# Performance work log

Hardware: AMD Instinct MI355X
Metric: run time of the kernel (lower is better)

The kernel has to match this reference:

```python
import jax, jax.numpy as jnp
import numpy as np
from jax import lax

DN = ('NCHW', 'OIHW', 'NCHW')

def conv(x, w, b, stride, pad):
    y = lax.conv_general_dilated(x, w, (stride, stride), [(pad, pad), (pad, pad)], dimension_numbers=DN)
    return y + b[None, :, None, None]

def setup_inputs() -> dict:
    key = jax.random.key(0)
    ks = jax.random.split(key, 16)
    s = 0.05
    inp = {
        'condition': jax.random.normal(ks[0], (16, 1, 256, 256), jnp.float32),
        'w1': jax.random.normal(ks[1], (64, 1, 4, 4), jnp.float32) * s,
        'b1': jnp.zeros((64,), jnp.float32),
        'w2': jax.random.normal(ks[2], (128, 64, 4, 4), jnp.float32) * s,
        'b2': jnp.zeros((128,), jnp.float32),
        'w3': jax.random.normal(ks[3], (128, 128, 3, 3), jnp.float32) * s,
        'b3': jnp.zeros((128,), jnp.float32),
        'r1w1': jax.random.normal(ks[4], (32, 128, 3, 3), jnp.float32) * s,
        'r1b1': jnp.zeros((32,), jnp.float32),
        'r1w2': jax.random.normal(ks[5], (128, 32, 1, 1), jnp.float32) * s,
        'r1b2': jnp.zeros((128,), jnp.float32),
        'r2w1': jax.random.normal(ks[6], (32, 128, 3, 3), jnp.float32) * s,
        'r2b1': jnp.zeros((32,), jnp.float32),
        'r2w2': jax.random.normal(ks[7], (128, 32, 1, 1), jnp.float32) * s,
        'r2b2': jnp.zeros((128,), jnp.float32),
        'wpre': jax.random.normal(ks[8], (4, 128, 1, 1), jnp.float32) * s,
        'bpre': jnp.zeros((4,), jnp.float32),
        'codebook': jax.random.normal(ks[9], (2048, 4), jnp.float32),
    }
    return inp

def reference(condition, w1, b1, w2, b2, w3, b3, r1w1, r1b1, r1w2, r1b2,
              r2w1, r2b1, r2w2, r2b2, wpre, bpre, codebook):
    # --- conv encoder (VQ-VAE standard) ---
    h = jax.nn.relu(conv(condition, w1, b1, 2, 1))   # [B,64,128,128]
    h = jax.nn.relu(conv(h, w2, b2, 2, 1))           # [B,128,64,64]
    h = conv(h, w3, b3, 1, 1)                        # [B,128,64,64]
    # residual stack: 2 blocks of relu->3x3->relu->1x1, residual add
    for wa, ba, wb, bb in ((r1w1, r1b1, r1w2, r1b2), (r2w1, r2b1, r2w2, r2b2)):
        t = conv(jax.nn.relu(h), wa, ba, 1, 1)
        t = conv(jax.nn.relu(t), wb, bb, 1, 0)
        h = h + t
    h = jax.nn.relu(h)
    z = conv(h, wpre, bpre, 1, 0)                    # [B,4,64,64]
    # --- cosine-distance vector quantization ---
    B, D, H, W = z.shape
    zf = jnp.transpose(z, (0, 2, 3, 1)).reshape(-1, D)          # [BHW, D]
    zn = zf / (jnp.linalg.norm(zf, axis=-1, keepdims=True) + 1e-12)
    en = codebook / (jnp.linalg.norm(codebook, axis=-1, keepdims=True) + 1e-12)
    sim = jnp.einsum('nd,kd->nk', zn, en)                       # cosine similarity
    idx = jnp.argmax(sim, axis=-1)                              # nearest code
    q = codebook[idx].reshape(B, H, W, D)
    c = jnp.transpose(q, (0, 3, 1, 2))                          # [B,4,64,64]
    return c
```

## Files before the change

kernel.cpp:

```cpp
#include <hip/hip_runtime.h>
#include <math.h>


typedef short v8s __attribute__((ext_vector_type(8)));
typedef float v4f __attribute__((ext_vector_type(4)));

#define B_OFF 4194304
#define A_OFF 12582912
#define W2_S 0
#define W3_S 393216
#define WR1_S 835584
#define WR2_S 946176
#define WP1_S 1056768
#define WP2_S 1069056

__device__ inline void limb3(float v, unsigned short& h, unsigned short& m,
                             unsigned short& l) {
    unsigned ub = __float_as_uint(v);
    unsigned hb = ub & 0xffff0000u;
    float r1 = v - __uint_as_float(hb);
    unsigned mb = __float_as_uint(r1) & 0xffff0000u;
    float r2 = r1 - __uint_as_float(mb);
    unsigned lb = __float_as_uint(r2) & 0xffff0000u;
    h = (unsigned short)(hb >> 16);
    m = (unsigned short)(mb >> 16);
    l = (unsigned short)(lb >> 16);
}

struct CfgConv2 {
    static constexpr int NC = 8, NT = 4, OC = 128, ICG = 64, IN_H = 128, IN_W = 128;
    static constexpr bool RELU_IN = false, RELU_OUT = true;
    __device__ static void tap(int c, int t, int& ry, int& rx) {
        int py = (c >> 2) & 1, px = (c >> 1) & 1;
        ry = (t >> 1) - py; rx = (t & 1) - px;
    }
    __device__ static void inaddr(int c, int oy, int r, int X,
                                  int& Yg, int& Xg, int& ic0) {
        int py = (c >> 2) & 1, px = (c >> 1) & 1;
        Yg = 2 * (oy + r - 1) + py; Xg = 2 * X + px; ic0 = (c & 1) * 32;
    }
    __device__ static int widx(int c, int t, int oc, int ic) {
        int py = (c >> 2) & 1, px = (c >> 1) & 1, half = c & 1;
        int dy = 2 * (t >> 1) + (1 - py), dx = 2 * (t & 1) + (1 - px);
        return ((oc * 64 + half * 32 + ic) * 4 + dy) * 4 + dx;
    }
};
struct CfgConv3 {
    static constexpr int NC = 4, NT = 9, OC = 128, ICG = 128, IN_H = 64, IN_W = 64;
    static constexpr bool RELU_IN = false, RELU_OUT = false;
    __device__ static void tap(int c, int t, int& ry, int& rx) {
        ry = t / 3 - 1; rx = t % 3 - 1;
    }
    __device__ static void inaddr(int c, int oy, int r, int X,
                                  int& Yg, int& Xg, int& ic0) {
        Yg = oy + r - 1; Xg = X; ic0 = c * 32;
    }
    __device__ static int widx(int c, int t, int oc, int ic) {
        return ((oc * 128 + c * 32 + ic) * 3 + t / 3) * 3 + t % 3;
    }
};
struct CfgRes {
    static constexpr int NC = 4, NT = 9, OC = 32, ICG = 128, IN_H = 64, IN_W = 64;
    __device__ static int widx(int c, int t, int oc, int ic) {
        return ((oc * 128 + c * 32 + ic) * 3 + t / 3) * 3 + t % 3;
    }
};
struct Cfg1x1 {
    static constexpr int NC = 1, NT = 1, OC = 128;
    __device__ static int widx(int c, int t, int oc, int ic) {
        return oc * 32 + ic;
    }
};

template <typename C>
__device__ inline void repack_one(const float* __restrict__ w,
                                  short* __restrict__ dst, int idx) {
    int s  = idx & 31;
    int oc = (idx >> 5) % C::OC;
    int ct = idx / (32 * C::OC);
    int c = ct / C::NT, t = ct % C::NT;
    float val = w[C::widx(c, t, oc, s)];
    unsigned short h, m, l;
    limb3(val, h, m, l);
    constexpr int NTILE = C::OC / 16;
    int nt = oc >> 4, o = oc & 15, q = s >> 3, j = s & 7;
    int fr = ((q * 16 + o) << 3) + j;
    dst[(((ct * 3 + 0) * NTILE + nt) << 9) + fr] = (short)h;
    dst[(((ct * 3 + 1) * NTILE + nt) << 9) + fr] = (short)m;
    dst[(((ct * 3 + 2) * NTILE + nt) << 9) + fr] = (short)l;
}

__global__ __launch_bounds__(256) void repack_all_k(
    const float* __restrict__ w2, const float* __restrict__ w3,
    const float* __restrict__ r1, const float* __restrict__ r2,
    const float* __restrict__ p1, const float* __restrict__ p2,
    short* __restrict__ base)
{
    int idx = blockIdx.x * 256 + threadIdx.x;
    if (idx < 131072) { repack_one<CfgConv2>(w2, base + W2_S, idx); return; }
    idx -= 131072;
    if (idx < 147456) { repack_one<CfgConv3>(w3, base + W3_S, idx); return; }
    idx -= 147456;
    if (idx < 36864)  { repack_one<CfgRes>(r1, base + WR1_S, idx); return; }
    idx -= 36864;
    if (idx < 36864)  { repack_one<CfgRes>(r2, base + WR2_S, idx); return; }
    idx -= 36864;
    if (idx < 4096)   { repack_one<Cfg1x1>(p1, base + WP1_S, idx); return; }
    idx -= 4096;
    if (idx < 4096)   { repack_one<Cfg1x1>(p2, base + WP2_S, idx); }
}

template <typename C>
__global__ __launch_bounds__(256, 3) void mfma_conv(
    const float* __restrict__ in, const short* __restrict__ repw,
    const float* __restrict__ bias, float* __restrict__ out, int n0)
{
    constexpr int APLANE = 3 * 66 * 32;
    constexpr int NTILE  = C::OC / 16;
    __shared__ __align__(16) short lA[3 * APLANE];

    int tid = threadIdx.x;
    int lane = tid & 63, wv = tid >> 6;
    int n_img = blockIdx.x >> 6, oy = blockIdx.x & 63;

    for (int idx = tid; idx < 3 * 3 * 2 * 16; idx += 256) {
        int plane = idx / 96;
        int rem = idx % 96;
        int rr = rem / 32;
        int hc = (rem / 16) & 1;
        int d = idx & 15;
        ((unsigned*)lA)[plane * 3168 + (rr * 66 + hc * 65) * 16 + d] = 0;
    }

    v4f acc[4][2] = {};
    int nbase = wv * 2;
    int Xq = tid & 15, icp = tid >> 4, quad = lane >> 4;

    float pv[24];
    auto issue_loads = [&](int c) {
#pragma unroll
        for (int it = 0; it < 12; it++) {
            int r = it >> 2, xg = it & 3;
            int X = xg * 16 + Xq;
            int Yg, Xg, ic0;
            C::inaddr(c, oy, r, X, Yg, Xg, ic0);
            float v0 = 0.f, v1 = 0.f;
            if (Yg >= 0 && Yg < C::IN_H) {
                int g = ((n_img * C::ICG + ic0 + 2 * icp) * C::IN_H + Yg) * C::IN_W + Xg;
                v0 = in[g];
                v1 = in[g + C::IN_H * C::IN_W];
            }
            pv[2 * it] = v0; pv[2 * it + 1] = v1;
        }
    };
    auto load_bf = [&](int c, int t, v8s (&dst)[2][3]) {
#pragma unroll
        for (int nt = 0; nt < 2; nt++)
#pragma unroll
            for (int L = 0; L < 3; L++)
                dst[nt][L] = *(const v8s*)(repw +
                    ((((c * C::NT + t) * 3 + L) * NTILE + (nbase + nt)) << 9) +
                    (lane << 3));
    };

    issue_loads(0);

    for (int c = 0; c < C::NC; c++) {
        __syncthreads();
#pragma unroll
        for (int it = 0; it < 12; it++) {
            int r = it >> 2, xg = it & 3;
            int X = xg * 16 + Xq;
            float v0 = pv[2 * it], v1 = pv[2 * it + 1];
            if constexpr (C::RELU_IN) { v0 = fmaxf(v0, 0.f); v1 = fmaxf(v1, 0.f); }
            unsigned short h0, m0, l0, h1, m1, l1;
            limb3(v0, h0, m0, l0);
            limb3(v1, h1, m1, l1);
            int cell = r * 66 + X + 1;
            int f = (cell + (cell >> 2)) & 3;
            int phys = (icp & 3) + 4 * (((icp >> 2) + f) & 3);
            unsigned* pa = (unsigned*)lA + cell * 16 + phys;
            pa[0]        = (unsigned)h0 | ((unsigned)h1 << 16);
            pa[3168]     = (unsigned)m0 | ((unsigned)m1 << 16);
            pa[2 * 3168] = (unsigned)l0 | ((unsigned)l1 << 16);
        }
        __syncthreads();
        if (c + 1 < C::NC) issue_loads(c + 1);

        v8s bf[2][2][3];
        load_bf(c, 0, bf[0]);
#pragma unroll
        for (int t = 0; t < C::NT; t++) {
            constexpr int NTT = C::NT;
            if (t + 1 < NTT) load_bf(c, t + 1, bf[(t + 1) & 1]);
            int ry, rx;
            C::tap(c, t, ry, rx);
#pragma unroll
            for (int mt = 0; mt < 4; mt++) {
                int x = mt * 16 + (lane & 15);
                int cell = (ry + 1) * 66 + (x + rx + 1);
                int f = (cell + (cell >> 2)) & 3;
                int aa = cell * 32 + (((quad + f) & 3) << 3);
                v8s ah = *(const v8s*)&lA[aa];
                v8s am = *(const v8s*)&lA[APLANE + aa];
                v8s al = *(const v8s*)&lA[2 * APLANE + aa];
#pragma unroll
                for (int nt = 0; nt < 2; nt++) {
                    v4f a0 = acc[mt][nt];
                    a0 = __builtin_amdgcn_mfma_f32_16x16x32_bf16(ah, bf[t & 1][nt][0], a0, 0, 0, 0);
                    a0 = __builtin_amdgcn_mfma_f32_16x16x32_bf16(ah, bf[t & 1][nt][1], a0, 0, 0, 0);
                    a0 = __builtin_amdgcn_mfma_f32_16x16x32_bf16(am, bf[t & 1][nt][0], a0, 0, 0, 0);
                    a0 = __builtin_amdgcn_mfma_f32_16x16x32_bf16(am, bf[t & 1][nt][1], a0, 0, 0, 0);
                    a0 = __builtin_amdgcn_mfma_f32_16x16x32_bf16(ah, bf[t & 1][nt][2], a0, 0, 0, 0);
                    a0 = __builtin_amdgcn_mfma_f32_16x16x32_bf16(al, bf[t & 1][nt][0], a0, 0, 0, 0);
                    acc[mt][nt] = a0;
                }
            }
        }
    }
#pragma unroll
    for (int mt = 0; mt < 4; mt++) {
        int x0 = mt * 16 + quad * 4;
#pragma unroll
        for (int nt = 0; nt < 2; nt++) {
            int oc = (nbase + nt) * 16 + (lane & 15);
            float bv = bias[oc];
            float v0 = acc[mt][nt][0] + bv;
            float v1 = acc[mt][nt][1] + bv;
            float v2 = acc[mt][nt][2] + bv;
            float v3 = acc[mt][nt][3] + bv;
            if constexpr (C::RELU_OUT) {
                v0 = fmaxf(v0, 0.f); v1 = fmaxf(v1, 0.f);
                v2 = fmaxf(v2, 0.f); v3 = fmaxf(v3, 0.f);
            }
            float4 o = make_float4(v0, v1, v2, v3);
            *(float4*)&out[(((n0 + n_img) * C::OC + oc) * 64 + oy) * 64 + x0] = o;
        }
    }
}

__global__ __launch_bounds__(256, 4) void mfma_res(
    const float* __restrict__ in, const short* __restrict__ repw,
    const float* __restrict__ b1, const short* __restrict__ repp,
    const float* __restrict__ b2, float* __restrict__ out)
{
    constexpr int APLANE = 3 * 66 * 32;
    __shared__ __align__(16) short lA[3 * APLANE];

    int tid = threadIdx.x;
    int lane = tid & 63, wv = tid >> 6;
    int n_img = blockIdx.x >> 6, oy = blockIdx.x & 63;

    for (int idx = tid; idx < 3 * 3 * 2 * 16; idx += 256) {
        int plane = idx / 96;
        int rem = idx % 96;
        int rr = rem / 32;
        int hc = (rem / 16) & 1;
        int d = idx & 15;
        ((unsigned*)lA)[plane * 3168 + (rr * 66 + hc * 65) * 16 + d] = 0;
    }

    v4f acc[2] = {};
    int Xq = tid & 15, icp = tid >> 4, quad = lane >> 4;

    float pv[24];
    auto issue_loads = [&](int c) {
#pragma unroll
        for (int it = 0; it < 12; it++) {
            int r = it >> 2, xg = it & 3;
            int X = xg * 16 + Xq;
            int Yg = oy + r - 1;
            float v0 = 0.f, v1 = 0.f;
            if (Yg >= 0 && Yg < 64) {
                int g = ((n_img * 128 + c * 32 + 2 * icp) * 64 + Yg) * 64 + X;
                v0 = in[g];
                v1 = in[g + 4096];
            }
            pv[2 * it] = v0; pv[2 * it + 1] = v1;
        }
    };

    issue_loads(0);

    for (int c = 0; c < 4; c++) {
        __syncthreads();
#pragma unroll
        for (int it = 0; it < 12; it++) {
            int r = it >> 2, xg = it & 3;
            int X = xg * 16 + Xq;
            float v0 = fmaxf(pv[2 * it], 0.f);
            float v1 = fmaxf(pv[2 * it + 1], 0.f);
            unsigned short h0, m0, l0, h1, m1, l1;
            limb3(v0, h0, m0, l0);
            limb3(v1, h1, m1, l1);
            int cell = r * 66 + X + 1;
            int f = (cell + (cell >> 2)) & 3;
            int phys = (icp & 3) + 4 * (((icp >> 2) + f) & 3);
            unsigned* pa = (unsigned*)lA + cell * 16 + phys;
            pa[0]        = (unsigned)h0 | ((unsigned)h1 << 16);
            pa[3168]     = (unsigned)m0 | ((unsigned)m1 << 16);
            pa[2 * 3168] = (unsigned)l0 | ((unsigned)l1 << 16);
        }
        __syncthreads();
        if (c + 1 < 4) issue_loads(c + 1);

        v8s bf[2][2][3];
        auto load_bf = [&](int t, v8s (&dst)[2][3]) {
#pragma unroll
            for (int nt = 0; nt < 2; nt++)
#pragma unroll
                for (int L = 0; L < 3; L++)
                    dst[nt][L] = *(const v8s*)(repw +
                        ((((c * 9 + t) * 3 + L) * 2 + nt) << 9) + (lane << 3));
        };
        load_bf(0, bf[0]);
#pragma unroll
        for (int t = 0; t < 9; t++) {
            if (t + 1 < 9) load_bf(t + 1, bf[(t + 1) & 1]);
            int ry = t / 3 - 1, rx = t % 3 - 1;
            int x = wv * 16 + (lane & 15);
            int cell = (ry + 1) * 66 + (x + rx + 1);
            int f = (cell + (cell >> 2)) & 3;
            int aa = cell * 32 + (((quad + f) & 3) << 3);
            v8s ah = *(const v8s*)&lA[aa];
            v8s am = *(const v8s*)&lA[APLANE + aa];
            v8s al = *(const v8s*)&lA[2 * APLANE + aa];
#pragma unroll
            for (int nt = 0; nt < 2; nt++) {
                v4f a0 = acc[nt];
                a0 = __builtin_amdgcn_mfma_f32_16x16x32_bf16(ah, bf[t & 1][nt][0], a0, 0, 0, 0);
                a0 = __builtin_amdgcn_mfma_f32_16x16x32_bf16(ah, bf[t & 1][nt][1], a0, 0, 0, 0);
                a0 = __builtin_amdgcn_mfma_f32_16x16x32_bf16(am, bf[t & 1][nt][0], a0, 0, 0, 0);
                a0 = __builtin_amdgcn_mfma_f32_16x16x32_bf16(am, bf[t & 1][nt][1], a0, 0, 0, 0);
                a0 = __builtin_amdgcn_mfma_f32_16x16x32_bf16(ah, bf[t & 1][nt][2], a0, 0, 0, 0);
                a0 = __builtin_amdgcn_mfma_f32_16x16x32_bf16(al, bf[t & 1][nt][0], a0, 0, 0, 0);
                acc[nt] = a0;
            }
        }
    }

    __syncthreads();
#pragma unroll
    for (int nt = 0; nt < 2; nt++) {
        int ic = nt * 16 + (lane & 15);
        int icp2 = ic >> 1, hilo = ic & 1;
        float bv = b1[ic];
#pragma unroll
        for (int r = 0; r < 4; r++) {
            int x = wv * 16 + quad * 4 + r;
            float v = fmaxf(acc[nt][r] + bv, 0.f);
            unsigned short h, m, l;
            limb3(v, h, m, l);
            int f = (x + (x >> 2)) & 3;
            int phys = (icp2 & 3) + 4 * (((icp2 >> 2) + f) & 3);
            int sa = x * 32 + phys * 2 + hilo;
            lA[sa] = (short)h;
            lA[2048 + sa] = (short)m;
            lA[4096 + sa] = (short)l;
        }
    }
    __syncthreads();

    v4f a2[8] = {};
    {
        int x = wv * 16 + (lane & 15);
        int f = (x + (x >> 2)) & 3;
        int aa = x * 32 + (((quad + f) & 3) << 3);
        v8s ah = *(const v8s*)&lA[aa];
        v8s am = *(const v8s*)&lA[2048 + aa];
        v8s al = *(const v8s*)&lA[4096 + aa];
#pragma unroll
        for (int nt = 0; nt < 8; nt++) {
            v8s bh = *(const v8s*)(repp + ((0 * 8 + nt) << 9) + (lane << 3));
            v8s bm = *(const v8s*)(repp + ((1 * 8 + nt) << 9) + (lane << 3));
            v8s bl = *(const v8s*)(repp + ((2 * 8 + nt) << 9) + (lane << 3));
            v4f a0 = a2[nt];
            a0 = __builtin_amdgcn_mfma_f32_16x16x32_bf16(ah, bh, a0, 0, 0, 0);
            a0 = __builtin_amdgcn_mfma_f32_16x16x32_bf16(ah, bm, a0, 0, 0, 0);
            a0 = __builtin_amdgcn_mfma_f32_16x16x32_bf16(am, bh, a0, 0, 0, 0);
            a0 = __builtin_amdgcn_mfma_f32_16x16x32_bf16(am, bm, a0, 0, 0, 0);
            a0 = __builtin_amdgcn_mfma_f32_16x16x32_bf16(ah, bl, a0, 0, 0, 0);
            a0 = __builtin_amdgcn_mfma_f32_16x16x32_bf16(al, bh, a0, 0, 0, 0);
            a2[nt] = a0;
        }
    }
#pragma unroll
    for (int nt = 0; nt < 8; nt++) {
        int oc = nt * 16 + (lane & 15);
        int x0 = wv * 16 + quad * 4;
        int off = ((n_img * 128 + oc) * 64 + oy) * 64 + x0;
        float4 hv = *(const float4*)&in[off];
        float bv = b2[oc];
        float4 o = make_float4(hv.x + a2[nt][0] + bv, hv.y + a2[nt][1] + bv,
                               hv.z + a2[nt][2] + bv, hv.w + a2[nt][3] + bv);
        *(float4*)&out[off] = o;
    }
}

__global__ __launch_bounds__(256) void conv1_k(
    const float* __restrict__ x, const float* __restrict__ w,
    const float* __restrict__ b, float* __restrict__ out)
{
    int tid = blockIdx.x * 256 + threadIdx.x;
    int n   = tid >> 14;
    int rem = tid & 16383;
    int oy  = rem >> 7;
    int ox  = rem & 127;
    int iy0 = oy * 2 - 1, ix0 = ox * 2 - 1;
    const float* xb = x + n * 65536;
    float v[16];
#pragma unroll
    for (int ky = 0; ky < 4; ky++) {
#pragma unroll
        for (int kx = 0; kx < 4; kx++) {
            int iy = iy0 + ky, ix = ix0 + kx;
            bool ok = (iy >= 0) & (iy < 256) & (ix >= 0) & (ix < 256);
            v[ky * 4 + kx] = ok ? xb[iy * 256 + ix] : 0.f;
        }
    }
    int obase = (n * 64) * 16384 + (oy << 7) + ox;
    for (int oc = 0; oc < 64; oc++) {
        float acc = b[oc];
        const float* wp = w + oc * 16;
#pragma unroll
        for (int k = 0; k < 16; k++) acc = fmaf(v[k], wp[k], acc);
        out[obase + oc * 16384] = fmaxf(acc, 0.f);
    }
}

__global__ __launch_bounds__(256) void prevq_k(
    const float* __restrict__ h, const float* __restrict__ wpre,
    const float* __restrict__ bpre, const float* __restrict__ cb,
    float* __restrict__ out)
{
    __shared__ float4 en[2048];
    for (int i = threadIdx.x; i < 2048; i += 256) {
        float c0 = cb[i * 4 + 0], c1 = cb[i * 4 + 1];
        float c2 = cb[i * 4 + 2], c3 = cb[i * 4 + 3];
        float nrm = sqrtf(c0 * c0 + c1 * c1 + c2 * c2 + c3 * c3) + 1e-12f;
        en[i] = make_float4(c0 / nrm, c1 / nrm, c2 / nrm, c3 / nrm);
    }
    __syncthreads();

    int tid = blockIdx.x * 256 + threadIdx.x;
    int n   = tid >> 12;
    int pos = tid & 4095;
    const float* hb = h + n * 128 * 4096 + pos;
    float z0 = bpre[0], z1 = bpre[1], z2 = bpre[2], z3 = bpre[3];
    for (int ic = 0; ic < 128; ic++) {
        float v = fmaxf(hb[ic * 4096], 0.f);
        z0 = fmaf(v, wpre[ic],       z0);
        z1 = fmaf(v, wpre[128 + ic], z1);
        z2 = fmaf(v, wpre[256 + ic], z2);
        z3 = fmaf(v, wpre[384 + ic], z3);
    }
    float best = -1e30f;
    int   bidx = 0;
    for (int k = 0; k < 2048; k++) {
        float4 e = en[k];
        float s = z0 * e.x + z1 * e.y + z2 * e.z + z3 * e.w;
        if (s > best) { best = s; bidx = k; }
    }
    const float* q = cb + bidx * 4;
    out[(n * 4 + 0) * 4096 + pos] = q[0];
    out[(n * 4 + 1) * 4096 + pos] = q[1];
    out[(n * 4 + 2) * 4096 + pos] = q[2];
    out[(n * 4 + 3) * 4096 + pos] = q[3];
}

extern "C" void kernel_launch(void* const* d_in, const int* in_sizes, int n_in,
                              void* d_out, int out_size, void* d_ws, size_t ws_size,
                              hipStream_t stream)
{
    const float* x    = (const float*)d_in[0];
    const float* w1   = (const float*)d_in[1];
    const float* b1   = (const float*)d_in[2];
    const float* w2   = (const float*)d_in[3];
    const float* b2   = (const float*)d_in[4];
    const float* w3   = (const float*)d_in[5];
    const float* b3   = (const float*)d_in[6];
    const float* r1w1 = (const float*)d_in[7];
    const float* r1b1 = (const float*)d_in[8];
    const float* r1w2 = (const float*)d_in[9];
    const float* r1b2 = (const float*)d_in[10];
    const float* r2w1 = (const float*)d_in[11];
    const float* r2b1 = (const float*)d_in[12];
    const float* r2w2 = (const float*)d_in[13];
    const float* r2b2 = (const float*)d_in[14];
    const float* wpre = (const float*)d_in[15];
    const float* bpre = (const float*)d_in[16];
    const float* cb   = (const float*)d_in[17];
    float* out = (float*)d_out;

    float* ws   = (float*)d_ws;
    short* wsS  = (short*)d_ws;
    float* B = ws + B_OFF;
    float* A = ws + A_OFF;

    repack_all_k<<<1408, 256, 0, stream>>>(w2, w3, r1w1, r2w1, r1w2, r2w2, wsS);

    conv1_k<<<512, 256, 0, stream>>>(x,               w1, b1, A);
    mfma_conv<CfgConv2><<<512, 256, 0, stream>>>(A, wsS + W2_S, b2, B, 0);
    conv1_k<<<512, 256, 0, stream>>>(x + 8 * 65536,   w1, b1, A);
    mfma_conv<CfgConv2><<<512, 256, 0, stream>>>(A, wsS + W2_S, b2, B, 8);

    mfma_conv<CfgConv3><<<1024, 256, 0, stream>>>(B, wsS + W3_S, b3, A, 0);

    mfma_res<<<1024, 256, 0, stream>>>(A, wsS + WR1_S, r1b1, wsS + WP1_S, r1b2, B);
    mfma_res<<<1024, 256, 0, stream>>>(B, wsS + WR2_S, r2b1, wsS + WP2_S, r2b2, A);

    prevq_k<<<256, 256, 0, stream>>>(A, wpre, bpre, cb, out);
}
```

Measured before the change: 485.0 us.

## Compute two output rows per block in residual conv kernel

Each residual-block kernel now handles two output rows per block instead of one. It loads a 4-row halo rather than 3 and splits waves into row/half-width tiles, so every wave reuses each loaded weight fragment across two M tiles. This cuts redundant halo input loads and per-block weight fetches, and halves the grid to 512 blocks. In exchange it uses more LDS and registers per block, and the occupancy hint in launch bounds is dropped.

```diff
diff --git a/kernel.cpp b/kernel.cpp
--- a/kernel.cpp
+++ b/kernel.cpp
@@ -239,37 +239,40 @@
     }
 }
 
-__global__ __launch_bounds__(256, 4) void mfma_res(
+__global__ __launch_bounds__(256) void mfma_res(
     const float* __restrict__ in, const short* __restrict__ repw,
     const float* __restrict__ b1, const short* __restrict__ repp,
     const float* __restrict__ b2, float* __restrict__ out)
 {
-    constexpr int APLANE = 3 * 66 * 32;
-    __shared__ __align__(16) short lA[3 * APLANE];
+    constexpr int PLANE_D = 4 * 66 * 16;
+    constexpr int PLANE_S = 2 * PLANE_D;
+    __shared__ __align__(16) short lA[3 * PLANE_S];
 
     int tid = threadIdx.x;
     int lane = tid & 63, wv = tid >> 6;
-    int n_img = blockIdx.x >> 6, oy = blockIdx.x & 63;
-
-    for (int idx = tid; idx < 3 * 3 * 2 * 16; idx += 256) {
-        int plane = idx / 96;
-        int rem = idx % 96;
+    int n_img = blockIdx.x >> 5;
+    int oy0 = (blockIdx.x & 31) << 1;
+    int jrow = wv >> 1, xh = wv & 1;
+
+    for (int idx = tid; idx < 3 * 4 * 2 * 16; idx += 256) {
+        int plane = idx / 128;
+        int rem = idx % 128;
         int rr = rem / 32;
-        int hc = (rem / 16) & 1;
+        int hc = (rem >> 4) & 1;
         int d = idx & 15;
-        ((unsigned*)lA)[plane * 3168 + (rr * 66 + hc * 65) * 16 + d] = 0;
-    }
-
-    v4f acc[2] = {};
+        ((unsigned*)lA)[plane * PLANE_D + (rr * 66 + hc * 65) * 16 + d] = 0;
+    }
+
+    v4f acc[2][2] = {};
     int Xq = tid & 15, icp = tid >> 4, quad = lane >> 4;
 
-    float pv[24];
+    float pv[32];
     auto issue_loads = [&](int c) {
 #pragma unroll
-        for (int it = 0; it < 12; it++) {
+        for (int it = 0; it < 16; it++) {
             int r = it >> 2, xg = it & 3;
             int X = xg * 16 + Xq;
-            int Yg = oy + r - 1;
+            int Yg = oy0 + r - 1;
             float v0 = 0.f, v1 = 0.f;
             if (Yg >= 0 && Yg < 64) {
                 int g = ((n_img * 128 + c * 32 + 2 * icp) * 64 + Yg) * 64 + X;
@@ -285,7 +288,7 @@
     for (int c = 0; c < 4; c++) {
         __syncthreads();
 #pragma unroll
-        for (int it = 0; it < 12; it++) {
+        for (int it = 0; it < 16; it++) {
             int r = it >> 2, xg = it & 3;
             int X = xg * 16 + Xq;
             float v0 = fmaxf(pv[2 * it], 0.f);
@@ -297,9 +300,9 @@
             int f = (cell + (cell >> 2)) & 3;
             int phys = (icp & 3) + 4 * (((icp >> 2) + f) & 3);
             unsigned* pa = (unsigned*)lA + cell * 16 + phys;
-            pa[0]        = (unsigned)h0 | ((unsigned)h1 << 16);
-            pa[3168]     = (unsigned)m0 | ((unsigned)m1 << 16);
-            pa[2 * 3168] = (unsigned)l0 | ((unsigned)l1 << 16);
+            pa[0]           = (unsigned)h0 | ((unsigned)h1 << 16);
+            pa[PLANE_D]     = (unsigned)m0 | ((unsigned)m1 << 16);
+            pa[2 * PLANE_D] = (unsigned)l0 | ((unsigned)l1 << 16);
         }
         __syncthreads();
         if (c + 1 < 4) issue_loads(c + 1);
@@ -318,57 +321,64 @@
         for (int t = 0; t < 9; t++) {
             if (t + 1 < 9) load_bf(t + 1, bf[(t + 1) & 1]);
             int ry = t / 3 - 1, rx = t % 3 - 1;
-            int x = wv * 16 + (lane & 15);
-            int cell = (ry + 1) * 66 + (x + rx + 1);
-            int f = (cell + (cell >> 2)) & 3;
-            int aa = cell * 32 + (((quad + f) & 3) << 3);
-            v8s ah = *(const v8s*)&lA[aa];
-            v8s am = *(const v8s*)&lA[APLANE + aa];
-            v8s al = *(const v8s*)&lA[2 * APLANE + aa];
-#pragma unroll
-            for (int nt = 0; nt < 2; nt++) {
-                v4f a0 = acc[nt];
-                a0 = __builtin_amdgcn_mfma_f32_16x16x32_bf16(ah, bf[t & 1][nt][0], a0, 0, 0, 0);
-                a0 = __builtin_amdgcn_mfma_f32_16x16x32_bf16(ah, bf[t & 1][nt][1], a0, 0, 0, 0);
-                a0 = __builtin_amdgcn_mfma_f32_16x16x32_bf16(am, bf[t & 1][nt][0], a0, 0, 0, 0);
-                a0 = __builtin_amdgcn_mfma_f32_16x16x32_bf16(am, bf[t & 1][nt][1], a0, 0, 0, 0);
-                a0 = __builtin_amdgcn_mfma_f32_16x16x32_bf16(ah, bf[t & 1][nt][2], a0, 0, 0, 0);
-                a0 = __builtin_amdgcn_mfma_f32_16x16x32_bf16(al, bf[t & 1][nt][0], a0, 0, 0, 0);
-                acc[nt] = a0;
+#pragma unroll
+            for (int mti = 0; mti < 2; mti++) {
+                int x = (xh * 2 + mti) * 16 + (lane & 15);
+                int cell = (jrow + ry + 1) * 66 + (x + rx + 1);
+                int f = (cell + (cell >> 2)) & 3;
+                int aa = cell * 32 + (((quad + f) & 3) << 3);
+                v8s ah = *(const v8s*)&lA[aa];
+                v8s am = *(const v8s*)&lA[PLANE_S + aa];
+                v8s al = *(const v8s*)&lA[2 * PLANE_S + aa];
+#pragma unroll
+                for (int nt = 0; nt < 2; nt++) {
+                    v4f a0 = acc[mti][nt];
+                    a0 = __builtin_amdgcn_mfma_f32_16x16x32_bf16(ah, bf[t & 1][nt][0], a0, 0, 0, 0);
+                    a0 = __builtin_amdgcn_mfma_f32_16x16x32_bf16(ah, bf[t & 1][nt][1], a0, 0, 0, 0);
+                    a0 = __builtin_amdgcn_mfma_f32_16x16x32_bf16(am, bf[t & 1][nt][0], a0, 0, 0, 0);
+                    a0 = __builtin_amdgcn_mfma_f32_16x16x32_bf16(am, bf[t & 1][nt][1], a0, 0, 0, 0);
+                    a0 = __builtin_amdgcn_mfma_f32_16x16x32_bf16(ah, bf[t & 1][nt][2], a0, 0, 0, 0);
+                    a0 = __builtin_amdgcn_mfma_f32_16x16x32_bf16(al, bf[t & 1][nt][0], a0, 0, 0, 0);
+                    acc[mti][nt] = a0;
+                }
             }
         }
     }
 
     __syncthreads();
 #pragma unroll
-    for (int nt = 0; nt < 2; nt++) {
-        int ic = nt * 16 + (lane & 15);
-        int icp2 = ic >> 1, hilo = ic & 1;
-        float bv = b1[ic];
-#pragma unroll
-        for (int r = 0; r < 4; r++) {
-            int x = wv * 16 + quad * 4 + r;
-            float v = fmaxf(acc[nt][r] + bv, 0.f);
-            unsigned short h, m, l;
-            limb3(v, h, m, l);
-            int f = (x + (x >> 2)) & 3;
-            int phys = (icp2 & 3) + 4 * (((icp2 >> 2) + f) & 3);
-            int sa = x * 32 + phys * 2 + hilo;
-            lA[sa] = (short)h;
-            lA[2048 + sa] = (short)m;
-            lA[4096 + sa] = (short)l;
+    for (int mti = 0; mti < 2; mti++) {
+#pragma unroll
+        for (int nt = 0; nt < 2; nt++) {
+            int ic = nt * 16 + (lane & 15);
+            int icp2 = ic >> 1, hilo = ic & 1;
+            float bv = b1[ic];
+#pragma unroll
+            for (int r = 0; r < 4; r++) {
+                int x = (xh * 2 + mti) * 16 + quad * 4 + r;
+                float v = fmaxf(acc[mti][nt][r] + bv, 0.f);
+                unsigned short h, m, l;
+                limb3(v, h, m, l);
+                int f = (x + (x >> 2)) & 3;
+                int phys = (icp2 & 3) + 4 * (((icp2 >> 2) + f) & 3);
+                int sa = x * 32 + phys * 2 + hilo;
+                lA[jrow * 6144 + sa]        = (short)h;
+                lA[jrow * 6144 + 2048 + sa] = (short)m;
+                lA[jrow * 6144 + 4096 + sa] = (short)l;
+            }
         }
     }
     __syncthreads();
 
-    v4f a2[8] = {};
-    {
+#pragma unroll
+    for (int j = 0; j < 2; j++) {
+        v4f a2[8] = {};
         int x = wv * 16 + (lane & 15);
         int f = (x + (x >> 2)) & 3;
         int aa = x * 32 + (((quad + f) & 3) << 3);
-        v8s ah = *(const v8s*)&lA[aa];
-        v8s am = *(const v8s*)&lA[2048 + aa];
-        v8s al = *(const v8s*)&lA[4096 + aa];
+        v8s ah = *(const v8s*)&lA[j * 6144 + aa];
+        v8s am = *(const v8s*)&lA[j * 6144 + 2048 + aa];
+        v8s al = *(const v8s*)&lA[j * 6144 + 4096 + aa];
 #pragma unroll
         for (int nt = 0; nt < 8; nt++) {
             v8s bh = *(const v8s*)(repp + ((0 * 8 + nt) << 9) + (lane << 3));
@@ -383,17 +393,17 @@
             a0 = __builtin_amdgcn_mfma_f32_16x16x32_bf16(al, bh, a0, 0, 0, 0);
             a2[nt] = a0;
         }
-    }
-#pragma unroll
-    for (int nt = 0; nt < 8; nt++) {
-        int oc = nt * 16 + (lane & 15);
-        int x0 = wv * 16 + quad * 4;
-        int off = ((n_img * 128 + oc) * 64 + oy) * 64 + x0;
-        float4 hv = *(const float4*)&in[off];
-        float bv = b2[oc];
-        float4 o = make_float4(hv.x + a2[nt][0] + bv, hv.y + a2[nt][1] + bv,
-                               hv.z + a2[nt][2] + bv, hv.w + a2[nt][3] + bv);
-        *(float4*)&out[off] = o;
+#pragma unroll
+        for (int nt = 0; nt < 8; nt++) {
+            int oc = nt * 16 + (lane & 15);
+            int x0 = wv * 16 + quad * 4;
+            int off = ((n_img * 128 + oc) * 64 + (oy0 + j)) * 64 + x0;
+            float4 hv = *(const float4*)&in[off];
+            float bv = b2[oc];
+            float4 o = make_float4(hv.x + a2[nt][0] + bv, hv.y + a2[nt][1] + bv,
+                                   hv.z + a2[nt][2] + bv, hv.w + a2[nt][3] + bv);
+            *(float4*)&out[off] = o;
+        }
     }
 }
 
@@ -506,8 +516,8 @@
 
     mfma_conv<CfgConv3><<<1024, 256, 0, stream>>>(B, wsS + W3_S, b3, A, 0);
 
-    mfma_res<<<1024, 256, 0, stream>>>(A, wsS + WR1_S, r1b1, wsS + WP1_S, r1b2, B);
-    mfma_res<<<1024, 256, 0, stream>>>(B, wsS + WR2_S, r2b1, wsS + WP2_S, r2b2, A);
+    mfma_res<<<512, 256, 0, stream>>>(A, wsS + WR1_S, r1b1, wsS + WP1_S, r1b2, B);
+    mfma_res<<<512, 256, 0, stream>>>(B, wsS + WR2_S, r2b1, wsS + WP2_S, r2b2, A);
 
     prevq_k<<<256, 256, 0, stream>>>(A, wpre, bpre, cb, out);
 }
```

After: 480.4 us. About the same (-0.9%).
